# Performance work log

Hardware: AMD Instinct MI355X
Metric: run time of the kernel (lower is better)

## Reference

```python
import jax, jax.numpy as jnp
import numpy as np
import math

D = 256        # input_size == d_k == d_v (per the module: d_k = input_size)
H = 4          # n_heads
MAX_LEN = 800  # PositionalEncoding max_len
NEG = float(-(2**32) + 1)
LN_EPS = 1e-5


def _make_pe():
    pe = np.zeros((MAX_LEN, D), dtype=np.float32)
    pos = np.arange(MAX_LEN, dtype=np.float32)[:, None]
    div = np.exp(np.arange(0, D, 2, dtype=np.float32) * -(math.log(10000.0) / D))
    pe[:, 0::2] = np.sin(pos * div)
    pe[:, 1::2] = np.cos(pos * div)
    return jnp.asarray(pe)


def setup_inputs() -> dict:
    key = jax.random.key(0)
    ks = jax.random.split(key, 12)
    B, L = 32, 512

    def xavier(k, shape):
        fan_in, fan_out = shape[0], shape[1]
        std = math.sqrt(2.0 / (fan_in + fan_out))
        return jax.random.normal(k, shape, dtype=jnp.float32) * std

    return {
        "Q": jax.random.normal(ks[0], (B, L, D), dtype=jnp.float32),
        "K": jax.random.normal(ks[1], (B, L, D), dtype=jnp.float32),
        "V": jax.random.normal(ks[2], (B, L, D), dtype=jnp.float32),
        "mask": jax.random.randint(ks[3], (B, L), 0, 2).astype(jnp.bool_),
        "pe": _make_pe(),
        "W_q": xavier(ks[4], (D, H * D)),
        "W_k": xavier(ks[5], (D, H * D)),
        "W_v": xavier(ks[6], (D, H * D)),
        "W_o": xavier(ks[7], (H * D, D)),
        "w1": xavier(ks[8], (D, D)),
        "b1": jnp.zeros((D,), dtype=jnp.float32),
        "w2": xavier(ks[9], (D, D)),
        "b2": jnp.zeros((D,), dtype=jnp.float32),
        "gamma": jnp.ones((D,), dtype=jnp.float32),
        "beta": jnp.zeros((D,), dtype=jnp.float32),
    }


def _layer_norm(x, gamma, beta):
    mu = jnp.mean(x, axis=-1, keepdims=True)
    var = jnp.mean(jnp.square(x - mu), axis=-1, keepdims=True)
    return (x - mu) * jax.lax.rsqrt(var + LN_EPS) * gamma + beta


def _mha(Q, K, V, mask, W_q, W_k, W_v, W_o):
    B, Lq, _ = Q.shape
    Lk = K.shape[1]

    def split_heads(X, W, L):
        # (B, L, D) @ (D, H*D) -> (B*H, L, D)
        return (X @ W).reshape(B, L, H, D).transpose(0, 2, 1, 3).reshape(B * H, L, D)

    Qh = split_heads(Q, W_q, Lq)
    Kh = split_heads(K, W_k, Lk)
    Vh = split_heads(V, W_v, Lk)

    scale = D ** 0.5 + 1e-6
    scores = jnp.einsum('bqd,bkd->bqk', Qh, Kh) / scale  # (B*H, Lq, Lk)

    pad = jnp.broadcast_to(mask[:, None, :], (B, H, Lq)).reshape(B * H, Lq)
    pad_mask = jnp.broadcast_to(pad[:, :, None], (B * H, Lq, Lk))
    causal = jnp.triu(jnp.ones((Lq, Lk), dtype=jnp.bool_), k=1)
    full_mask = causal[None] | pad_mask
    scores = jnp.where(full_mask, NEG, scores)

    att = jax.nn.softmax(scores, axis=-1)
    Vatt = jnp.einsum('bqk,bkd->bqd', att, Vh)  # (B*H, Lq, D)
    Vatt = Vatt.reshape(B, H, Lq, D).transpose(0, 2, 1, 3).reshape(B, Lq, H * D)
    return Vatt @ W_o


def reference(Q, K, V, mask, pe, W_q, W_k, W_v, W_o, w1, b1, w2, b2, gamma, beta):
    Lq, Lk, Lv = Q.shape[1], K.shape[1], V.shape[1]
    Qp = Q + pe[None, :Lq]
    Kp = K + pe[None, :Lk]
    Vp = V + pe[None, :Lv]

    Vatt = _mha(Qp, Kp, Vp, mask, W_q, W_k, W_v, W_o)
    X = _layer_norm(Qp + Vatt, gamma, beta)
    ffn = jax.nn.relu(X @ w1.T + b1) @ w2.T + b2
    return _layer_norm(ffn + X, gamma, beta)
```

## Files before the change

### kernel.cpp

```cpp
#include <hip/hip_runtime.h>
#include <stdint.h>

#define SEQ   512
#define DM    256
#define NB    32
#define NH    4
#define HD    (NH * DM)
#define PE_MASK (SEQ * DM - 1)
#define NEGV  (-4294967295.0f)

typedef __attribute__((ext_vector_type(8))) short short8;
typedef __attribute__((ext_vector_type(4))) float f32x4;

#if defined(__has_builtin)
#if __has_builtin(__builtin_amdgcn_global_load_lds)
#define HAS_ASYNC 1
#endif
#endif
#ifndef HAS_ASYNC
#define HAS_ASYNC 0
#endif

__device__ __forceinline__ float b2f(unsigned short u) {
    return __uint_as_float(((uint32_t)u) << 16);
}
__device__ __forceinline__ unsigned short f2b(float f) {
    uint32_t u = __float_as_uint(f);
    u += 0x7fffu + ((u >> 16) & 1u);
    return (unsigned short)(u >> 16);
}
__device__ __forceinline__ float fast_exp2(float x) {
    float r;
    asm("v_exp_f32 %0, %1" : "=v"(r) : "v"(x));
    return r;
}

__device__ __forceinline__ int swzb(int b) {
    return b ^ (((b >> 7) & 7) << 4);
}

__global__ __launch_bounds__(256) void prep_all(
    const unsigned char* __restrict__ mask_raw, int* __restrict__ maskc,
    const float* __restrict__ Wq, const float* __restrict__ Wk,
    const float* __restrict__ Wv, unsigned short* __restrict__ WqT,
    const float* __restrict__ Wo, unsigned short* __restrict__ WoT,
    const float* __restrict__ w1, const float* __restrict__ w2,
    unsigned short* __restrict__ o1, unsigned short* __restrict__ o2,
    const float* __restrict__ Q, const float* __restrict__ K,
    const float* __restrict__ V, const float* __restrict__ pe,
    unsigned short* __restrict__ Qp, unsigned short* __restrict__ Kp,
    unsigned short* __restrict__ Vp)
{
    __shared__ unsigned short tile[32][33];
    __shared__ int enc[2];
    const int blk = blockIdx.x;
    const int tid = threadIdx.x;

    if (blk < 64) {
        if (tid == 0) { enc[0] = 0; enc[1] = 0; }
        __syncthreads();
        if (tid < 255 && mask_raw[tid * 4 + 1]) atomicOr(&enc[0], 1);
        if (tid < 128 && ((const int*)mask_raw)[tid * 2 + 1]) atomicOr(&enc[1], 1);
        __syncthreads();
        int i = blk * 256 + tid;
        int v;
        if (enc[0])      v = (mask_raw[i] != 0);
        else if (enc[1]) v = (((const int*)mask_raw)[i] != 0);
        else             v = ((((const int*)mask_raw)[i * 2] |
                              ((const int*)mask_raw)[i * 2 + 1]) != 0);
        maskc[i] = v;
    } else if (blk < 832) {
        int t = blk - 64;
        int x = t & 31, y = (t >> 5) & 7, zz = t >> 8;
        const float* in = (zz == 0) ? Wq : (zz == 1) ? Wk : Wv;
        unsigned short* op = WqT + (long)zz * 262144;
        int r0 = y * 32, c0 = x * 32;
        int i = tid >> 3, j = (tid & 7) * 4;
        float4 v = *reinterpret_cast<const float4*>(in + (long)(r0 + i) * HD + c0 + j);
        tile[i][j + 0] = f2b(v.x); tile[i][j + 1] = f2b(v.y);
        tile[i][j + 2] = f2b(v.z); tile[i][j + 3] = f2b(v.w);
        __syncthreads();
        ushort4 w;
        w.x = tile[j + 0][i]; w.y = tile[j + 1][i];
        w.z = tile[j + 2][i]; w.w = tile[j + 3][i];
        *reinterpret_cast<ushort4*>(op + (long)(c0 + i) * DM + r0 + j) = w;
    } else if (blk < 1088) {
        int t = blk - 832;
        int x = t & 7, y = t >> 3;
        int r0 = y * 32, c0 = x * 32;
        int i = tid >> 3, j = (tid & 7) * 4;
        float4 v = *reinterpret_cast<const float4*>(Wo + (long)(r0 + i) * DM + c0 + j);
        tile[i][j + 0] = f2b(v.x); tile[i][j + 1] = f2b(v.y);
        tile[i][j + 2] = f2b(v.z); tile[i][j + 3] = f2b(v.w);
        __syncthreads();
        ushort4 w;
        w.x = tile[j + 0][i]; w.y = tile[j + 1][i];
        w.z = tile[j + 2][i]; w.w = tile[j + 3][i];
        *reinterpret_cast<ushort4*>(WoT + (long)(c0 + i) * HD + r0 + j) = w;
    } else if (blk < 1216) {
        int t = blk - 1088;
        const float* in = (t < 64) ? w1 : w2;
        unsigned short* out = (t < 64) ? o1 : o2;
        long i = (long)((t & 63) * 256 + tid) * 4;
        float4 x = *reinterpret_cast<const float4*>(in + i);
        ushort4 o;
        o.x = f2b(x.x); o.y = f2b(x.y); o.z = f2b(x.z); o.w = f2b(x.w);
        *reinterpret_cast<ushort4*>(out + i) = o;
    } else {
        int t = blk - 1216;
        int seg = t >> 12;
        const float* X = (seg == 0) ? Q : (seg == 1) ? K : V;
        unsigned short* O = (seg == 0) ? Qp : (seg == 1) ? Kp : Vp;
        long i = (long)((t & 4095) * 256 + tid) * 4;
        float4 x = *reinterpret_cast<const float4*>(X + i);
        float4 p = *reinterpret_cast<const float4*>(pe + (i & PE_MASK));
        ushort4 o;
        o.x = f2b(x.x + p.x); o.y = f2b(x.y + p.y);
        o.z = f2b(x.z + p.z); o.w = f2b(x.w + p.w);
        *reinterpret_cast<ushort4*>(O + i) = o;
    }
}

__global__ __launch_bounds__(256) void tv_kernel(
    const unsigned short* __restrict__ Vh, unsigned short* __restrict__ VhT,
    float* __restrict__ part, int nbl)
{
    __shared__ unsigned short tile[32][33];
    const int blk = blockIdx.x;
    const int tid = threadIdx.x;
    const int nT = nbl * NH * 128;

    if (blk < nT) {
        int x = blk & 7, y = (blk >> 3) & 15, zz = blk >> 7;
        int b = zz / NH, hh = zz % NH;
        const unsigned short* ip = Vh + (long)b * SEQ * HD + (long)hh * DM;
        unsigned short* op = VhT + (long)b * SEQ * HD + (long)hh * SEQ * DM;
        int r0 = y * 32, c0 = x * 32;
        int i = tid >> 3, j = (tid & 7) * 4;
        ushort4 v = *reinterpret_cast<const ushort4*>(ip + (long)(r0 + i) * HD + c0 + j);
        tile[i][j + 0] = v.x; tile[i][j + 1] = v.y;
        tile[i][j + 2] = v.z; tile[i][j + 3] = v.w;
        __syncthreads();
        ushort4 w;
        w.x = tile[j + 0][i]; w.y = tile[j + 1][i];
        w.z = tile[j + 2][i]; w.w = tile[j + 3][i];
        *reinterpret_cast<ushort4*>(op + (long)(c0 + i) * SEQ + r0 + j) = w;
    } else {
        int t = blk - nT;
        int bl = t >> 3, seg = t & 7;
        const unsigned short* p = Vh + (long)bl * SEQ * HD + (long)seg * 64 * HD;
        int c = tid * 4;
        float s0 = 0.f, s1 = 0.f, s2 = 0.f, s3 = 0.f;
        for (int l = 0; l < 64; ++l) {
            ushort4 v = *reinterpret_cast<const ushort4*>(p + (long)l * HD + c);
            s0 += b2f(v.x); s1 += b2f(v.y); s2 += b2f(v.z); s3 += b2f(v.w);
        }
        float4 o = {s0, s1, s2, s3};
        *reinterpret_cast<float4*>(part + (long)(bl * 8 + seg) * HD + c) = o;
    }
}

template<bool BIAS, bool RELU, bool OUTBF16>
__global__ __launch_bounds__(256) void gemm_bt(
    const unsigned short* __restrict__ A, int lda,
    const unsigned short* __restrict__ B, int ldb,
    void* __restrict__ Cv, int ldc,
    const float* __restrict__ bias, float scale, int K, int Hdiv,
    long sAb, long sAh, long sAz,
    long sBb, long sBh, long sBz,
    long sCb, long sCh, long sCz)
{
    const int m0 = blockIdx.y * 128;
    const int n0 = blockIdx.x * 128;
    int z  = blockIdx.z;
    int bb = z / Hdiv, hh = z % Hdiv;
    const unsigned short* Ab = A + bb * sAb + hh * sAh + (long)z * sAz;
    const unsigned short* Bb = B + bb * sBb + hh * sBh + (long)z * sBz;
    long coff = bb * sCb + hh * sCh + (long)z * sCz;
    const float scl = (z == 0) ? scale : 1.0f;

    __shared__ unsigned short As[128 * 32];
    __shared__ unsigned short Bs[128 * 32];

    const int tid  = threadIdx.x;
    const int lane = tid & 63;
    const int wave = tid >> 6;
    const int wm   = (wave >> 1) * 64;
    const int wn   = (wave & 1) * 64;
    const int lm   = lane & 15;
    const int kq   = (lane >> 4) * 8;

    f32x4 acc[4][4] = {};

    for (int k0 = 0; k0 < K; k0 += 32) {
#pragma unroll
        for (int it = 0; it < 2; ++it) {
            int id = tid + it * 256;
            int r  = id >> 2;
            int c8 = (id & 3) * 8;
            const unsigned short* gA = Ab + (long)(m0 + r) * lda + k0 + c8;
            const unsigned short* gB = Bb + (long)(n0 + r) * ldb + k0 + c8;
#if HAS_ASYNC
            unsigned short* lA = &As[(size_t)(it * 256 + wave * 64) * 8];
            unsigned short* lB = &Bs[(size_t)(it * 256 + wave * 64) * 8];
            __builtin_amdgcn_global_load_lds(
                (const __attribute__((address_space(1))) void*)gA,
                (__attribute__((address_space(3))) void*)lA, 16, 0, 0);
            __builtin_amdgcn_global_load_lds(
                (const __attribute__((address_space(1))) void*)gB,
                (__attribute__((address_space(3))) void*)lB, 16, 0, 0);
#else
            *reinterpret_cast<uint4*>(&As[(size_t)id * 8]) =
                *reinterpret_cast<const uint4*>(gA);
            *reinterpret_cast<uint4*>(&Bs[(size_t)id * 8]) =
                *reinterpret_cast<const uint4*>(gB);
#endif
        }
        __syncthreads();

        short8 af[4], bfr[4];
#pragma unroll
        for (int i = 0; i < 4; ++i)
            af[i] = *reinterpret_cast<const short8*>(&As[(wm + i * 16 + lm) * 32 + kq]);
#pragma unroll
        for (int j = 0; j < 4; ++j)
            bfr[j] = *reinterpret_cast<const short8*>(&Bs[(wn + j * 16 + lm) * 32 + kq]);
#pragma unroll
        for (int i = 0; i < 4; ++i)
#pragma unroll
            for (int j = 0; j < 4; ++j)
                acc[i][j] = __builtin_amdgcn_mfma_f32_16x16x32_bf16(af[i], bfr[j], acc[i][j], 0, 0, 0);
        __syncthreads();
    }

#pragma unroll
    for (int j = 0; j < 4; ++j) {
        int col  = n0 + wn + j * 16 + lm;
        float bv = 0.f;
        if (BIAS) bv = bias[col];
#pragma unroll
        for (int i = 0; i < 4; ++i) {
#pragma unroll
            for (int r = 0; r < 4; ++r) {
                int row = m0 + wm + i * 16 + (lane >> 4) * 4 + r;
                float v = acc[i][j][r] * scl + bv;
                if (RELU) v = fmaxf(v, 0.f);
                long idx = coff + (long)row * ldc + col;
                if (OUTBF16) reinterpret_cast<unsigned short*>(Cv)[idx] = f2b(v);
                else         reinterpret_cast<float*>(Cv)[idx] = v;
            }
        }
    }
}

__device__ __forceinline__ void stage_k32(
    unsigned short* __restrict__ buf, const unsigned short* __restrict__ Ak,
    int kc, int qt, int tid, int wave)
{
    for (int it = 0; it <= qt; ++it) {
        int id = tid + it * 256;
#if HAS_ASYNC
        int U = swzb(id * 16);
        const unsigned short* g = Ak + (long)(U >> 6) * HD + kc * 32 + ((U >> 4) & 3) * 8;
        unsigned short* l = buf + (size_t)(it * 256 + wave * 64) * 8;
        __builtin_amdgcn_global_load_lds(
            (const __attribute__((address_space(1))) void*)g,
            (__attribute__((address_space(3))) void*)l, 16, 0, 0);
#else
        const unsigned short* g = Ak + (long)(id >> 2) * HD + kc * 32 + (id & 3) * 8;
        *reinterpret_cast<uint4*>((char*)buf + swzb(id * 16)) =
            *reinterpret_cast<const uint4*>(g);
#endif
    }
}

__device__ __forceinline__ void stage_v64(
    unsigned short* __restrict__ buf, const unsigned short* __restrict__ Av,
    int c64, int tid, int wave)
{
#pragma unroll
    for (int it = 0; it < 8; ++it) {
        int id = tid + it * 256;
#if HAS_ASYNC
        int U = swzb(id * 16);
        const unsigned short* g = Av + (long)(U >> 7) * SEQ + c64 * 64 + ((U >> 4) & 7) * 8;
        unsigned short* l = buf + (size_t)(it * 256 + wave * 64) * 8;
        __builtin_amdgcn_global_load_lds(
            (const __attribute__((address_space(1))) void*)g,
            (__attribute__((address_space(3))) void*)l, 16, 0, 0);
#else
        const unsigned short* g = Av + (long)(id >> 3) * SEQ + c64 * 64 + (id & 7) * 8;
        *reinterpret_cast<uint4*>((char*)buf + swzb(id * 16)) =
            *reinterpret_cast<const uint4*>(g);
#endif
    }
}

__global__ __launch_bounds__(256, 2) void flash_attn(
    const unsigned short* __restrict__ Qh,
    const unsigned short* __restrict__ Kh,
    const unsigned short* __restrict__ VhT,
    const float* __restrict__ part,
    unsigned short* __restrict__ Vatt,
    const int* __restrict__ maskc, int bh0, int nbh)
{
    const int tid  = threadIdx.x;
    const int lane = tid & 63;
    const int wave = tid >> 6;
    const int lm   = lane & 15;
    const int qg   = lane >> 4;
    const int kq   = qg * 8;

    const int L = blockIdx.x;
    int z, qt;
    if ((nbh & 7) == 0) {
        int x = L & 7, m = L >> 3;
        int mq = m & 7;
        qt = (mq & 1) ? (7 - (mq >> 1)) : (mq >> 1);
        z  = x + 8 * (m >> 3);
    } else {
        z = L % nbh; qt = L / nbh;
    }
    const int b_l = z >> 2, h = z & 3;
    const int m0  = qt * 64;
    const int wq0 = m0 + wave * 16;
    const long qkbase = (long)b_l * SEQ * HD + (long)h * DM;
    const unsigned short* Aq = Qh + qkbase;
    const unsigned short* Ak = Kh + qkbase;
    const unsigned short* Av = VhT + (long)b_l * SEQ * HD + (long)h * SEQ * DM;
    unsigned short* Ov = Vatt + qkbase;
    const int bglob = (bh0 + z) >> 2;

    __shared__ unsigned short Ks[2 * SEQ * 32];
    __shared__ __align__(16) unsigned short Pw[4][16][40];

    f32x4 S[32] = {};
    const int NT = (m0 >> 4) + wave + 1;

    stage_k32(Ks, Ak, 0, qt, tid, wave);
    __syncthreads();
    for (int kc = 0; kc < 8; ++kc) {
        unsigned short* cur = (kc & 1) ? (Ks + SEQ * 32) : Ks;
        unsigned short* nxt = (kc & 1) ? Ks : (Ks + SEQ * 32);
        short8 qf = *reinterpret_cast<const short8*>(
            Aq + (long)(wq0 + lm) * HD + kc * 32 + kq);
        if (kc < 7) {
            stage_k32(nxt, Ak, kc + 1, qt, tid, wave);
        } else {
            stage_v64(Ks, Av, 0, tid, wave);
        }
        __builtin_amdgcn_s_setprio(1);
#pragma unroll
        for (int nt = 0; nt < 32; ++nt) {
            if (nt < NT) {
                int row = nt * 16 + lm;
                short8 bf = *reinterpret_cast<const short8*>(
                    (const char*)cur + swzb(row * 64 + qg * 16));
                S[nt] = __builtin_amdgcn_mfma_f32_16x16x32_bf16(qf, bf, S[nt], 0, 0, 0);
            }
        }
        __builtin_amdgcn_s_setprio(0);
        __syncthreads();
    }

    int   qrow[4];
    bool  rowm[4];
    float mx[4], sm[4];
#pragma unroll
    for (int r = 0; r < 4; ++r) {
        int q = wq0 + qg * 4 + r;
        qrow[r] = q;
        rowm[r] = maskc[bglob * SEQ + q] != 0;
        mx[r] = -3.4e38f;
    }
#pragma unroll
    for (int nt = 0; nt < 32; ++nt) {
        int k = nt * 16 + lm;
#pragma unroll
        for (int r = 0; r < 4; ++r) {
            float v = S[nt][r];
            if (k > qrow[r]) v = NEGV;
            S[nt][r] = v;
            mx[r] = fmaxf(mx[r], v);
        }
    }
#pragma unroll
    for (int r = 0; r < 4; ++r) {
#pragma unroll
        for (int off = 8; off >= 1; off >>= 1)
            mx[r] = fmaxf(mx[r], __shfl_xor(mx[r], off));
        sm[r] = 0.f;
    }
    uint32_t pk[32][2];
#pragma unroll
    for (int nt = 0; nt < 32; ++nt) {
        float e0 = fast_exp2(S[nt][0] - mx[0]);
        float e1 = fast_exp2(S[nt][1] - mx[1]);
        float e2 = fast_exp2(S[nt][2] - mx[2]);
        float e3 = fast_exp2(S[nt][3] - mx[3]);
        sm[0] += e0; sm[1] += e1; sm[2] += e2; sm[3] += e3;
        pk[nt][0] = (uint32_t)f2b(e0) | ((uint32_t)f2b(e1) << 16);
        pk[nt][1] = (uint32_t)f2b(e2) | ((uint32_t)f2b(e3) << 16);
    }
#pragma unroll
    for (int r = 0; r < 4; ++r) {
#pragma unroll
        for (int off = 8; off >= 1; off >>= 1)
            sm[r] += __shfl_xor(sm[r], off);
        sm[r] = 1.0f / sm[r];
    }

    unsigned short* Vb0 = Ks;
    unsigned short* Vb1 = Ks + 16384;
    const int NC = qt + 1;
    f32x4 O[16] = {};
#pragma unroll
    for (int c64 = 0; c64 < 8; ++c64) {
        if (c64 < NC) {
            unsigned short* Vcur = (c64 & 1) ? Vb1 : Vb0;
            __syncthreads();
            if (c64 + 1 < NC) {
                unsigned short* Vnext = (c64 & 1) ? Vb0 : Vb1;
                stage_v64(Vnext, Av, c64 + 1, tid, wave);
            }
#pragma unroll
            for (int t = 0; t < 2; ++t) {
#pragma unroll
                for (int tt = 0; tt < 2; ++tt) {
                    int nt = c64 * 4 + t * 2 + tt;
#pragma unroll
                    for (int r = 0; r < 4; ++r)
                        Pw[wave][qg * 4 + r][tt * 16 + lm] =
                            (unsigned short)(pk[nt][r >> 1] >> ((r & 1) * 16));
                }
                short8 pf = *reinterpret_cast<const short8*>(&Pw[wave][lm][kq]);
                __builtin_amdgcn_s_setprio(1);
#pragma unroll
                for (int nt2 = 0; nt2 < 16; ++nt2) {
                    int row = nt2 * 16 + lm;
                    short8 vf = *reinterpret_cast<const short8*>(
                        (const char*)Vcur + swzb(row * 128 + t * 64 + qg * 16));
                    O[nt2] = __builtin_amdgcn_mfma_f32_16x16x32_bf16(pf, vf, O[nt2], 0, 0, 0);
                }
                __builtin_amdgcn_s_setprio(0);
            }
        }
    }

    const float* pb = part + (long)(b_l * 8) * HD + h * DM + lm;
    float vmf[16];
#pragma unroll
    for (int nt2 = 0; nt2 < 16; ++nt2) {
        float s = 0.f;
#pragma unroll
        for (int seg = 0; seg < 8; ++seg)
            s += pb[(long)seg * HD + nt2 * 16];
        vmf[nt2] = s * (1.0f / SEQ);
    }
#pragma unroll
    for (int nt2 = 0; nt2 < 16; ++nt2) {
#pragma unroll
        for (int r = 0; r < 4; ++r) {
            int l = wq0 + qg * 4 + r;
            float val = rowm[r] ? vmf[nt2] : O[nt2][r] * sm[r];
            Ov[(long)l * HD + nt2 * 16 + lm] = f2b(val);
        }
    }
}

__global__ __launch_bounds__(256) void ln1_kernel(
    const unsigned short* __restrict__ AttO, const float* __restrict__ Q,
    const float* __restrict__ pe,
    const float* __restrict__ gamma, const float* __restrict__ beta,
    float* __restrict__ outf, unsigned short* __restrict__ outb)
{
    int row  = blockIdx.x * 4 + (threadIdx.x >> 6);
    int lane = threadIdx.x & 63;
    long base = (long)row * DM + lane * 4;
    ushort4 a = *reinterpret_cast<const ushort4*>(AttO + base);
    float4 qv = *reinterpret_cast<const float4*>(Q + base);
    float4 pv = *reinterpret_cast<const float4*>(pe + (base & PE_MASK));
    float x[4] = {b2f(a.x) + qv.x + pv.x, b2f(a.y) + qv.y + pv.y,
                  b2f(a.z) + qv.z + pv.z, b2f(a.w) + qv.w + pv.w};
    float s = x[0] + x[1] + x[2] + x[3];
#pragma unroll
    for (int off = 32; off > 0; off >>= 1) s += __shfl_xor(s, off);
    float mu = s * (1.0f / DM);
    float vs = 0.f;
#pragma unroll
    for (int t = 0; t < 4; ++t) { float d = x[t] - mu; vs += d * d; }
#pragma unroll
    for (int off = 32; off > 0; off >>= 1) vs += __shfl_xor(vs, off);
    float inv = rsqrtf(vs * (1.0f / DM) + 1e-5f);
    int d0 = lane * 4;
    float4 g = *reinterpret_cast<const float4*>(gamma + d0);
    float4 bt = *reinterpret_cast<const float4*>(beta + d0);
    float4 o;
    o.x = (x[0] - mu) * inv * g.x + bt.x;
    o.y = (x[1] - mu) * inv * g.y + bt.y;
    o.z = (x[2] - mu) * inv * g.z + bt.z;
    o.w = (x[3] - mu) * inv * g.w + bt.w;
    *reinterpret_cast<float4*>(outf + base) = o;
    ushort4 ob;
    ob.x = f2b(o.x); ob.y = f2b(o.y); ob.z = f2b(o.z); ob.w = f2b(o.w);
    *reinterpret_cast<ushort4*>(outb + base) = ob;
}

__global__ __launch_bounds__(256) void ln2_kernel(
    const float* __restrict__ F, const float* __restrict__ X,
    const float* __restrict__ gamma, const float* __restrict__ beta,
    float* __restrict__ out)
{
    int row  = blockIdx.x * 4 + (threadIdx.x >> 6);
    int lane = threadIdx.x & 63;
    long base = (long)row * DM + lane * 4;
    float4 a = *reinterpret_cast<const float4*>(F + base);
    float4 c = *reinterpret_cast<const float4*>(X + base);
    float x[4] = {a.x + c.x, a.y + c.y, a.z + c.z, a.w + c.w};
    float s = x[0] + x[1] + x[2] + x[3];
#pragma unroll
    for (int off = 32; off > 0; off >>= 1) s += __shfl_xor(s, off);
    float mu = s * (1.0f / DM);
    float vs = 0.f;
#pragma unroll
    for (int t = 0; t < 4; ++t) { float d = x[t] - mu; vs += d * d; }
#pragma unroll
    for (int off = 32; off > 0; off >>= 1) vs += __shfl_xor(vs, off);
    float inv = rsqrtf(vs * (1.0f / DM) + 1e-5f);
    int d0 = lane * 4;
    float4 g = *reinterpret_cast<const float4*>(gamma + d0);
    float4 bt = *reinterpret_cast<const float4*>(beta + d0);
    float4 o;
    o.x = (x[0] - mu) * inv * g.x + bt.x;
    o.y = (x[1] - mu) * inv * g.y + bt.y;
    o.z = (x[2] - mu) * inv * g.z + bt.z;
    o.w = (x[3] - mu) * inv * g.w + bt.w;
    *reinterpret_cast<float4*>(out + base) = o;
}

extern "C" void kernel_launch(void* const* d_in, const int* in_sizes, int n_in,
                              void* d_out, int out_size, void* d_ws, size_t ws_size,
                              hipStream_t stream)
{
    const float* Q  = (const float*)d_in[0];
    const float* Ki = (const float*)d_in[1];
    const float* Vi = (const float*)d_in[2];
    const unsigned char* mask_raw = (const unsigned char*)d_in[3];
    const float* pe = (const float*)d_in[4];
    const float* Wq = (const float*)d_in[5];
    const float* Wk = (const float*)d_in[6];
    const float* Wv = (const float*)d_in[7];
    const float* Wo = (const float*)d_in[8];
    const float* w1 = (const float*)d_in[9];
    const float* b1 = (const float*)d_in[10];
    const float* w2 = (const float*)d_in[11];
    const float* b2 = (const float*)d_in[12];
    const float* gamma = (const float*)d_in[13];
    const float* beta  = (const float*)d_in[14];
    float* out = (float*)d_out;

    const size_t MiB = 1048576;
    char* ws = (char*)d_ws;

    int CB = 1;
    for (int cb = 32; cb >= 1; cb >>= 1) {
        size_t scr_sz = (size_t)(5 * cb) * MiB + (size_t)cb * 32768;
        if (scr_sz < 24 * MiB) scr_sz = 24 * MiB;
        if ((59 * MiB + scr_sz) <= ws_size) { CB = cb; break; }
    }
    const int NCH = NB / CB;

    unsigned short* WqT  = (unsigned short*)(ws);
    unsigned short* WkT  = WqT + 262144;
    unsigned short* WvT  = WkT + 262144;
    unsigned short* WoT  = WvT + 262144;
    unsigned short* w1b  = (unsigned short*)(ws + 2 * MiB);
    unsigned short* w2b  = w1b + 65536;
    int*            maskc = (int*)(ws + 2 * MiB + 262144);
    unsigned short* Qp   = (unsigned short*)(ws + 3 * MiB);
    unsigned short* Kp   = (unsigned short*)(ws + 11 * MiB);
    unsigned short* Vp   = (unsigned short*)(ws + 19 * MiB);
    unsigned short* AttO = (unsigned short*)(ws + 27 * MiB);
    unsigned short* Xb   = (unsigned short*)(ws + 35 * MiB);
    float*          Xf   = (float*)(ws + 43 * MiB);
    char*           scr  = ws + 59 * MiB;
    unsigned short* Qh   = (unsigned short*)(scr);
    unsigned short* Kh   = (unsigned short*)(scr + (size_t)CB * MiB);
    unsigned short* Vh   = (unsigned short*)(scr + (size_t)2 * CB * MiB);
    unsigned short* VhT  = (unsigned short*)(scr + (size_t)3 * CB * MiB);
    unsigned short* Vatt = (unsigned short*)(scr + (size_t)4 * CB * MiB);
    float*          part = (float*)(scr + (size_t)5 * CB * MiB);
    unsigned short* H1   = (unsigned short*)(scr);
    float*          Ff   = (float*)(scr + 8 * MiB);

    const float SCALE_Q = (float)((1.0 / (16.0 + 1e-6)) * 1.4426950408889634);
    const long CROWS = (long)CB * SEQ;
    const long CBELT = (long)CB * MiB / 2;

    prep_all<<<13504, 256, 0, stream>>>(
        mask_raw, maskc, Wq, Wk, Wv, WqT, Wo, WoT,
        w1, w2, w1b, w2b, Q, Ki, Vi, pe, Qp, Kp, Vp);

    for (int c = 0; c < NCH; ++c) {
        const long r0   = (long)c * CROWS;
        const int  bh0  = c * CB * NH;
        const int  gy   = (int)(CROWS / 128);
        const int  nbh  = CB * NH;

        gemm_bt<false, false, true><<<dim3(8, gy, 3), 256, 0, stream>>>(
            Qp + r0 * DM, DM, WqT, DM, Qh, HD, nullptr, SCALE_Q, DM,
            1, 4194304, 0, 0, 262144, 0, 0, CBELT, 0, 0);

        tv_kernel<<<CB * NH * 128 + CB * 8, 256, 0, stream>>>(
            Vh, VhT, part, CB);

        flash_attn<<<dim3(8 * nbh, 1, 1), 256, 0, stream>>>(
            Qh, Kh, VhT, part, Vatt, maskc, bh0, nbh);

        gemm_bt<false, false, true><<<dim3(2, gy, 1), 256, 0, stream>>>(
            Vatt, HD, WoT, HD, AttO + r0 * DM, DM, nullptr, 1.f, HD,
            1, 0,0,0, 0,0,0, 0,0,0);
    }

    ln1_kernel<<<4096, 256, 0, stream>>>(AttO, Q, pe, gamma, beta, Xf, Xb);

    gemm_bt<true, true, true><<<dim3(2, 128, 1), 256, 0, stream>>>(
        Xb, DM, w1b, DM, H1, DM, b1, 1.f, DM, 1, 0,0,0, 0,0,0, 0,0,0);
    gemm_bt<true, false, false><<<dim3(2, 128, 1), 256, 0, stream>>>(
        H1, DM, w2b, DM, Ff, DM, b2, 1.f, DM, 1, 0,0,0, 0,0,0, 0,0,0);

    ln2_kernel<<<4096, 256, 0, stream>>>(Ff, Xf, gamma, beta, out);
}
```

Measured before the change: 332.6 us.

## Double-buffer LDS tiles in gemm_bt and swizzle LDS layout

Splits the GEMM shared-memory tiles into two buffers so the next K-slice loads while MFMAs run on the current one, cutting the loop to one barrier per iteration. It also applies an XOR-style swizzle (swzb) to LDS addresses to reduce bank conflicts on the fragment reads. The cost is twice the LDS per block, which may lower occupancy. It depends on swzb being defined elsewhere and on the swizzle matching between async writes and reads.

```diff
diff --git a/kernel.cpp b/kernel.cpp
--- a/kernel.cpp
+++ b/kernel.cpp
@@ -179,8 +179,8 @@
     long coff = bb * sCb + hh * sCh + (long)z * sCz;
     const float scl = (z == 0) ? scale : 1.0f;
 
-    __shared__ unsigned short As[128 * 32];
-    __shared__ unsigned short Bs[128 * 32];
+    __shared__ unsigned short As[2][128 * 32];
+    __shared__ unsigned short Bs[2][128 * 32];
 
     const int tid  = threadIdx.x;
     const int lane = tid & 63;
@@ -192,17 +192,18 @@
 
     f32x4 acc[4][4] = {};
 
-    for (int k0 = 0; k0 < K; k0 += 32) {
+    auto stage = [&](int b, int k0) {
 #pragma unroll
         for (int it = 0; it < 2; ++it) {
             int id = tid + it * 256;
-            int r  = id >> 2;
-            int c8 = (id & 3) * 8;
+#if HAS_ASYNC
+            int U  = swzb(id * 16);
+            int r  = U >> 6;
+            int c8 = ((U >> 4) & 3) * 8;
             const unsigned short* gA = Ab + (long)(m0 + r) * lda + k0 + c8;
             const unsigned short* gB = Bb + (long)(n0 + r) * ldb + k0 + c8;
-#if HAS_ASYNC
-            unsigned short* lA = &As[(size_t)(it * 256 + wave * 64) * 8];
-            unsigned short* lB = &Bs[(size_t)(it * 256 + wave * 64) * 8];
+            unsigned short* lA = &As[b][(size_t)(it * 256 + wave * 64) * 8];
+            unsigned short* lB = &Bs[b][(size_t)(it * 256 + wave * 64) * 8];
             __builtin_amdgcn_global_load_lds(
                 (const __attribute__((address_space(1))) void*)gA,
                 (__attribute__((address_space(3))) void*)lA, 16, 0, 0);
@@ -210,21 +211,35 @@
                 (const __attribute__((address_space(1))) void*)gB,
                 (__attribute__((address_space(3))) void*)lB, 16, 0, 0);
 #else
-            *reinterpret_cast<uint4*>(&As[(size_t)id * 8]) =
+            int r  = id >> 2;
+            int c8 = (id & 3) * 8;
+            const unsigned short* gA = Ab + (long)(m0 + r) * lda + k0 + c8;
+            const unsigned short* gB = Bb + (long)(n0 + r) * ldb + k0 + c8;
+            *reinterpret_cast<uint4*>((char*)As[b] + swzb(id * 16)) =
                 *reinterpret_cast<const uint4*>(gA);
-            *reinterpret_cast<uint4*>(&Bs[(size_t)id * 8]) =
+            *reinterpret_cast<uint4*>((char*)Bs[b] + swzb(id * 16)) =
                 *reinterpret_cast<const uint4*>(gB);
 #endif
         }
-        __syncthreads();
+    };
+
+    stage(0, 0);
+    __syncthreads();
+    const int nk = K >> 5;
+    for (int kk = 0; kk < nk; ++kk) {
+        const int cur = kk & 1;
+        if (kk + 1 < nk)
+            stage(cur ^ 1, (kk + 1) * 32);
 
         short8 af[4], bfr[4];
 #pragma unroll
         for (int i = 0; i < 4; ++i)
-            af[i] = *reinterpret_cast<const short8*>(&As[(wm + i * 16 + lm) * 32 + kq]);
+            af[i] = *reinterpret_cast<const short8*>(
+                (const char*)As[cur] + swzb((wm + i * 16 + lm) * 64 + kq * 2));
 #pragma unroll
         for (int j = 0; j < 4; ++j)
-            bfr[j] = *reinterpret_cast<const short8*>(&Bs[(wn + j * 16 + lm) * 32 + kq]);
+            bfr[j] = *reinterpret_cast<const short8*>(
+                (const char*)Bs[cur] + swzb((wn + j * 16 + lm) * 64 + kq * 2));
 #pragma unroll
         for (int i = 0; i < 4; ++i)
 #pragma unroll
```

After: 324.7 us. 1.02x faster.
